# Optimization experiments

Hardware: AMD Instinct MI355X
Metric: run time of the kernel (lower is better)

Reference implementation:

```python
import jax, jax.numpy as jnp
import numpy as np

N_USERS, N_ITEMS, N_ENT = 2500, 3000, 2500
N = N_USERS + N_ITEMS + N_ENT
D, NREL, L, K, NH = 128, 32, 2, 16, 2
NE = 256_000
F_MOVIE, F_USER = 768, 512
GATE_T = 0.5


def _lin(x, w, b):
    return x @ w + b


def setup_inputs() -> dict:
    key = jax.random.key(0)
    ks = iter(jax.random.split(key, 64))
    def rn(shape, s=0.05):
        return jax.random.normal(next(ks), shape, jnp.float32) * s
    def zb():
        return jnp.zeros((D,), jnp.float32)
    inp = dict(
        user_w=rn((N_USERS, D), 0.1), item_w=rn((N_ITEMS, D), 0.1),
        ent_w=rn((N_ENT, D), 0.1), rel_w=rn((NREL, D), 0.1),
        mfeat=rn((N_ITEMS, F_MOVIE), 1.0), ufeat=rn((N_USERS, F_USER), 1.0),
        me_w1=rn((F_MOVIE, D)), me_b1=zb(), me_w2=rn((D, D)), me_b2=zb(),
        ue_w1=rn((F_USER, D)), ue_b1=zb(), ue_w2=rn((D, D)), ue_b2=zb(),
        cm_qw=rn((D, D)), cm_qb=zb(), cm_kw=rn((D, D)), cm_kb=zb(),
        cm_vw=rn((D, D)), cm_vb=zb(), cm_ow=rn((D, D)), cm_ob=zb(),
        mg_w=rn((2 * D, D)), mg_b=zb(), ug_w=rn((2 * D, D)), ug_b=zb(),
        gnn_qw=rn((L, D, D)), gnn_qb=jnp.zeros((L, D), jnp.float32),
        gnn_kw=rn((L, D, D)), gnn_kb=jnp.zeros((L, D), jnp.float32),
        gnn_vw=rn((L, D, D)), gnn_vb=jnp.zeros((L, D), jnp.float32),
        la_w=rn(((L + 1) * D, D)), la_b=zb(),
        adj_data=jax.random.uniform(next(ks), (NE,), jnp.float32, 1e-3, 1.0),
        adj_row=jax.random.randint(next(ks), (NE,), 0, N),
        adj_col=jax.random.randint(next(ks), (NE,), 0, N),
    )
    return inp


def _forward(user_w, item_w, ent_w, rel_w, mfeat, ufeat,
             me_w1, me_b1, me_w2, me_b2, ue_w1, ue_b1, ue_w2, ue_b2,
             cm_qw, cm_qb, cm_kw, cm_kb, cm_vw, cm_vb, cm_ow, cm_ob,
             mg_w, mg_b, ug_w, ug_b,
             gnn_qw, gnn_qb, gnn_kw, gnn_kb, gnn_vw, gnn_vb,
             la_w, la_b, adj_data, adj_row, adj_col):
    hd = D // NH
    # --- modality encoders (dropout is inference-mode identity) ---
    mm_item = jax.nn.relu(_lin(jax.nn.relu(_lin(mfeat, me_w1, me_b1)), me_w2, me_b2))
    mm_user = jax.nn.relu(_lin(jax.nn.relu(_lin(ufeat, ue_w1, ue_b1)), ue_w2, ue_b2))
    # --- MultiHeadCrossModalAttention(mm_item, mm_item): 2 modalities ---
    x = jnp.stack([mm_item, mm_item], axis=1)                     # [B, 2, D]
    B, M = x.shape[0], x.shape[1]
    q = _lin(x, cm_qw, cm_qb).reshape(B, M, NH, hd).transpose(0, 2, 1, 3)
    k = _lin(x, cm_kw, cm_kb).reshape(B, M, NH, hd).transpose(0, 2, 1, 3)
    v = _lin(x, cm_vw, cm_vb).reshape(B, M, NH, hd).transpose(0, 2, 1, 3)
    attn = jax.nn.softmax(jnp.einsum('bhmd,bhnd->bhmn', q, k) / jnp.sqrt(jnp.float32(hd)), axis=-1)
    ao = jnp.einsum('bhmn,bhnd->bhmd', attn, v).transpose(0, 2, 1, 3).reshape(B, M, D)
    mm_item = _lin(ao, cm_ow, cm_ob).sum(axis=1)                  # [B, D]
    # --- gated fusion (NOTE: double sigmoid, faithful to source) ---
    mg = jax.nn.sigmoid(jax.nn.sigmoid(_lin(jnp.concatenate([item_w, mm_item], axis=-1), mg_w, mg_b)) / GATE_T)
    fused_item = mg * item_w + (1.0 - mg) * mm_item + 0.1 * item_w
    ug = jax.nn.sigmoid(jax.nn.sigmoid(_lin(jnp.concatenate([user_w, mm_user], axis=-1), ug_w, ug_b)) / GATE_T)
    fused_user = ug * user_w + (1.0 - ug) * mm_user + 0.1 * user_w
    # --- GNN propagation with SparseKnowledgeAttention ---
    emb = jnp.concatenate([fused_user, fused_item, ent_w], axis=0)  # [N, D]
    rel_mean = rel_w.mean(axis=0)                                  # [D]
    embs = [emb]
    for l in range(L):
        e = embs[-1]
        # sparse adj @ e via gather + segment_sum
        side = jax.ops.segment_sum(adj_data[:, None] * e[adj_col], adj_row, num_segments=N)
        qn = _lin(e, gnn_qw[l], gnn_qb[l])
        kn = _lin(side * rel_mean[None, :], gnn_kw[l], gnn_kb[l])
        scores = (qn @ kn.T) / jnp.sqrt(jnp.float32(D))            # [N, N]
        tv, ti = jax.lax.top_k(scores, K)                          # [N, K]
        w = jax.nn.softmax(tv, axis=-1)
        vn = _lin(side, gnn_vw[l], gnn_vb[l])
        agg = jnp.einsum('nk,nkd->nd', w, vn[ti])                  # gather + weighted sum
        embs.append(jax.nn.relu(agg))
    final = _lin(jnp.concatenate(embs, axis=-1), la_w, la_b)       # layer_agg on stacked layers
    def _norm(z):
        return z / jnp.maximum(jnp.linalg.norm(z, axis=1, keepdims=True), 1e-12)
    return (_norm(final[:N_USERS]),
            _norm(final[N_USERS:N_USERS + N_ITEMS]),
            item_w, mm_item)


def reference(user_w, item_w, ent_w, rel_w, mfeat, ufeat,
              me_w1, me_b1, me_w2, me_b2, ue_w1, ue_b1, ue_w2, ue_b2,
              cm_qw, cm_qb, cm_kw, cm_kb, cm_vw, cm_vb, cm_ow, cm_ob,
              mg_w, mg_b, ug_w, ug_b,
              gnn_qw, gnn_qb, gnn_kw, gnn_kb, gnn_vw, gnn_vb,
              la_w, la_b, adj_data, adj_row, adj_col):
    return _forward(user_w, item_w, ent_w, rel_w, mfeat, ufeat,
                    me_w1, me_b1, me_w2, me_b2, ue_w1, ue_b1, ue_w2, ue_b2,
                    cm_qw, cm_qb, cm_kw, cm_kb, cm_vw, cm_vb, cm_ow, cm_ob,
                    mg_w, mg_b, ug_w, ug_b,
                    gnn_qw, gnn_qb, gnn_kw, gnn_kb, gnn_vw, gnn_vb,
                    la_w, la_b, adj_data, adj_row, adj_col)
```

## Files before the change

kernel.cpp:

```cpp
#include <hip/hip_runtime.h>
#include <hip/hip_bf16.h>
#include <math.h>

#define N_USERS 2500
#define N_ITEMS 3000
#define N_ENT   2500
#define NTOT    8000
#define D       128
#define NEDGE   256000
#define NSLICE  8
#define NMAT    12

typedef unsigned short u16;
typedef unsigned int u32;
typedef unsigned long long u64;
typedef __attribute__((ext_vector_type(8))) short short8;
typedef __attribute__((ext_vector_type(4))) float f32x4;

static __device__ __forceinline__ u16 bf16bits(float x) {
  __hip_bfloat16 h = __float2bfloat16(x);
  return *reinterpret_cast<u16*>(&h);
}

struct WsplitArgs {
  const float* w[NMAT];
  int useks[NMAT];
  int K[NMAT];
  int cum[NMAT + 1];
  int ofs[NMAT];
};

__global__ void k_wsplit_all(WsplitArgs a, const float* __restrict__ relmean,
                             u16* __restrict__ arena) {
  const int e = blockIdx.x * 256 + threadIdx.x;
  if (e >= a.cum[NMAT]) return;
  int i = 0;
  while (e >= a.cum[i + 1]) ++i;
  const int local = e - a.cum[i];
  const int k = local >> 7, j = local & 127;
  const int K = a.K[i];
  float x = a.w[i][(size_t)k * 128 + j];
  if (a.useks[i]) x *= relmean[k];
  const __hip_bfloat16 h1 = __float2bfloat16(x);
  const float r1 = x - __bfloat162float(h1);
  const __hip_bfloat16 h2 = __float2bfloat16(r1);
  const float r2 = r1 - __bfloat162float(h2);
  const __hip_bfloat16 h3 = __float2bfloat16(r2);
  u16* __restrict__ base = arena + a.ofs[i] + (size_t)j * K + k;
  base[0]               = *(const u16*)&h1;
  base[(size_t)128 * K] = *(const u16*)&h2;
  base[(size_t)256 * K] = *(const u16*)&h3;
}

static __device__ __forceinline__ void gemm3_core(const float* __restrict__ A,
                                                  const u16* __restrict__ wsg,
                                                  const float* __restrict__ b,
                                                  float* __restrict__ out,
                                                  u16* __restrict__ ob,
                                                  int M, int K, int mode,
                                                  int bid, int tid) {
  const int lane = tid & 63;
  const int wave = tid >> 6;
  const int rbase = bid * 64 + wave * 16;
  const int colL = lane & 15;
  const int kofs = (lane >> 4) * 8;

  f32x4 acc[8];
#pragma unroll
  for (int ct = 0; ct < 8; ++ct) acc[ct] = (f32x4){0.f, 0.f, 0.f, 0.f};

  const int arow = (rbase + colL < M) ? (rbase + colL) : (M - 1);
  const float* __restrict__ arp = A + (size_t)arow * K;

  for (int k0 = 0; k0 < K; k0 += 32) {
    const float4 f0 = *(const float4*)(arp + k0 + kofs);
    const float4 f1 = *(const float4*)(arp + k0 + kofs + 4);
    float av[8] = {f0.x, f0.y, f0.z, f0.w, f1.x, f1.y, f1.z, f1.w};
    short8 a1, a2, a3;
#pragma unroll
    for (int e = 0; e < 8; ++e) {
      const float x = av[e];
      const __hip_bfloat16 h1 = __float2bfloat16(x);
      const float r1 = x - __bfloat162float(h1);
      const __hip_bfloat16 h2 = __float2bfloat16(r1);
      const float r2 = r1 - __bfloat162float(h2);
      const __hip_bfloat16 h3 = __float2bfloat16(r2);
      a1[e] = *(const short*)&h1;
      a2[e] = *(const short*)&h2;
      a3[e] = *(const short*)&h3;
    }
#pragma unroll
    for (int ct = 0; ct < 8; ++ct) {
      const int j = ct * 16 + colL;
      const u16* wp = wsg + (size_t)j * K + k0 + kofs;
      const short8 b1 = *(const short8*)wp;
      const short8 b2 = *(const short8*)(wp + (size_t)128 * K);
      const short8 b3 = *(const short8*)(wp + (size_t)256 * K);
      acc[ct] = __builtin_amdgcn_mfma_f32_16x16x32_bf16(a1, b1, acc[ct], 0, 0, 0);
      acc[ct] = __builtin_amdgcn_mfma_f32_16x16x32_bf16(a1, b2, acc[ct], 0, 0, 0);
      acc[ct] = __builtin_amdgcn_mfma_f32_16x16x32_bf16(a2, b1, acc[ct], 0, 0, 0);
      acc[ct] = __builtin_amdgcn_mfma_f32_16x16x32_bf16(a2, b2, acc[ct], 0, 0, 0);
      acc[ct] = __builtin_amdgcn_mfma_f32_16x16x32_bf16(a1, b3, acc[ct], 0, 0, 0);
      acc[ct] = __builtin_amdgcn_mfma_f32_16x16x32_bf16(a3, b1, acc[ct], 0, 0, 0);
    }
  }

#pragma unroll
  for (int ct = 0; ct < 8; ++ct) {
    const int j = ct * 16 + colL;
    const float bj = b[j];
#pragma unroll
    for (int r = 0; r < 4; ++r) {
      const int row = rbase + (lane >> 4) * 4 + r;
      if (row < M) {
        float c = acc[ct][r] + bj;
        if (mode == 1) c = fmaxf(c, 0.f);
        else if (mode == 2) c *= 2.f;
        out[(size_t)row * 128 + j] = c;
        if (ob) ob[(size_t)row * 128 + j] = bf16bits(c);
      }
    }
  }
}

static __device__ __forceinline__ void gemm3x2_core(const float* __restrict__ A,
                                                    const u16* __restrict__ wsgA,
                                                    const float* __restrict__ bA,
                                                    float* __restrict__ outA,
                                                    u16* __restrict__ obA,
                                                    const u16* __restrict__ wsgB,
                                                    const float* __restrict__ bB,
                                                    float* __restrict__ outB,
                                                    int M, int K, int bid, int tid) {
  const int lane = tid & 63;
  const int wave = tid >> 6;
  const int rbase = bid * 64 + wave * 16;
  const int colL = lane & 15;
  const int kofs = (lane >> 4) * 8;

  f32x4 accA[8], accB[8];
#pragma unroll
  for (int ct = 0; ct < 8; ++ct) {
    accA[ct] = (f32x4){0.f, 0.f, 0.f, 0.f};
    accB[ct] = (f32x4){0.f, 0.f, 0.f, 0.f};
  }

  const int arow = (rbase + colL < M) ? (rbase + colL) : (M - 1);
  const float* __restrict__ arp = A + (size_t)arow * K;

  for (int k0 = 0; k0 < K; k0 += 32) {
    const float4 f0 = *(const float4*)(arp + k0 + kofs);
    const float4 f1 = *(const float4*)(arp + k0 + kofs + 4);
    float av[8] = {f0.x, f0.y, f0.z, f0.w, f1.x, f1.y, f1.z, f1.w};
    short8 a1, a2, a3;
#pragma unroll
    for (int e = 0; e < 8; ++e) {
      const float x = av[e];
      const __hip_bfloat16 h1 = __float2bfloat16(x);
      const float r1 = x - __bfloat162float(h1);
      const __hip_bfloat16 h2 = __float2bfloat16(r1);
      const float r2 = r1 - __bfloat162float(h2);
      const __hip_bfloat16 h3 = __float2bfloat16(r2);
      a1[e] = *(const short*)&h1;
      a2[e] = *(const short*)&h2;
      a3[e] = *(const short*)&h3;
    }
#pragma unroll
    for (int ct = 0; ct < 8; ++ct) {
      const int j = ct * 16 + colL;
      {
        const u16* wp = wsgA + (size_t)j * K + k0 + kofs;
        const short8 b1 = *(const short8*)wp;
        const short8 b2 = *(const short8*)(wp + (size_t)128 * K);
        const short8 b3 = *(const short8*)(wp + (size_t)256 * K);
        accA[ct] = __builtin_amdgcn_mfma_f32_16x16x32_bf16(a1, b1, accA[ct], 0, 0, 0);
        accA[ct] = __builtin_amdgcn_mfma_f32_16x16x32_bf16(a1, b2, accA[ct], 0, 0, 0);
        accA[ct] = __builtin_amdgcn_mfma_f32_16x16x32_bf16(a2, b1, accA[ct], 0, 0, 0);
        accA[ct] = __builtin_amdgcn_mfma_f32_16x16x32_bf16(a2, b2, accA[ct], 0, 0, 0);
        accA[ct] = __builtin_amdgcn_mfma_f32_16x16x32_bf16(a1, b3, accA[ct], 0, 0, 0);
        accA[ct] = __builtin_amdgcn_mfma_f32_16x16x32_bf16(a3, b1, accA[ct], 0, 0, 0);
      }
      {
        const u16* wp = wsgB + (size_t)j * K + k0 + kofs;
        const short8 b1 = *(const short8*)wp;
        const short8 b2 = *(const short8*)(wp + (size_t)128 * K);
        const short8 b3 = *(const short8*)(wp + (size_t)256 * K);
        accB[ct] = __builtin_amdgcn_mfma_f32_16x16x32_bf16(a1, b1, accB[ct], 0, 0, 0);
        accB[ct] = __builtin_amdgcn_mfma_f32_16x16x32_bf16(a1, b2, accB[ct], 0, 0, 0);
        accB[ct] = __builtin_amdgcn_mfma_f32_16x16x32_bf16(a2, b1, accB[ct], 0, 0, 0);
        accB[ct] = __builtin_amdgcn_mfma_f32_16x16x32_bf16(a2, b2, accB[ct], 0, 0, 0);
        accB[ct] = __builtin_amdgcn_mfma_f32_16x16x32_bf16(a1, b3, accB[ct], 0, 0, 0);
        accB[ct] = __builtin_amdgcn_mfma_f32_16x16x32_bf16(a3, b1, accB[ct], 0, 0, 0);
      }
    }
  }

#pragma unroll
  for (int ct = 0; ct < 8; ++ct) {
    const int j = ct * 16 + colL;
    const float bjA = bA[j];
    const float bjB = bB[j];
#pragma unroll
    for (int r = 0; r < 4; ++r) {
      const int row = rbase + (lane >> 4) * 4 + r;
      if (row < M) {
        const float cA = accA[ct][r] + bjA;
        outA[(size_t)row * 128 + j] = cA;
        obA[(size_t)row * 128 + j] = bf16bits(cA);
        outB[(size_t)row * 128 + j] = accB[ct][r] + bjB;
      }
    }
  }
}

__global__ __launch_bounds__(256) void k_gemm3(const float* __restrict__ A,
                                               const u16* __restrict__ wsg,
                                               const float* __restrict__ b,
                                               float* __restrict__ out,
                                               u16* __restrict__ ob,
                                               int M, int K, int mode) {
  gemm3_core(A, wsg, b, out, ob, M, K, mode, blockIdx.x, threadIdx.x);
}

__global__ __launch_bounds__(256) void k_gemm3b(const float* A0, const u16* w0,
                                                const float* b0, float* o0, int M0, int K0, int nb0,
                                                const float* A1, const u16* w1,
                                                const float* b1, float* o1, int M1, int K1,
                                                int mode) {
  if ((int)blockIdx.x < nb0)
    gemm3_core(A0, w0, b0, o0, nullptr, M0, K0, mode, blockIdx.x, threadIdx.x);
  else
    gemm3_core(A1, w1, b1, o1, nullptr, M1, K1, mode, blockIdx.x - nb0, threadIdx.x);
}

__global__ __launch_bounds__(256) void k_gemm3qkv(const float* e, const u16* wq,
                                                  const float* bq, float* qn, u16* qb,
                                                  const float* side, const u16* wk,
                                                  const float* bk, float* kn, u16* kb,
                                                  const u16* wv, const float* bv, float* vn,
                                                  int M, int nb0) {
  if ((int)blockIdx.x < nb0)
    gemm3_core(e, wq, bq, qn, qb, M, 128, 0, blockIdx.x, threadIdx.x);
  else
    gemm3x2_core(side, wk, bk, kn, kb, wv, bv, vn, M, 128, blockIdx.x - nb0, threadIdx.x);
}

static __device__ __forceinline__ void gemm3w_core(const float* __restrict__ A,
                                                   const u16* __restrict__ wsg,
                                                   const float* __restrict__ b,
                                                   float* __restrict__ out,
                                                   int M, int K, int mode,
                                                   int bid, int tid) {
  const int lane = tid & 63;
  const int wave = tid >> 6;
  const int rbase = bid * 32 + (wave & 1) * 16;
  const int ct0  = (wave >> 1) * 4;
  const int colL = lane & 15;
  const int kofs = (lane >> 4) * 8;

  f32x4 acc[4];
#pragma unroll
  for (int ct = 0; ct < 4; ++ct) acc[ct] = (f32x4){0.f, 0.f, 0.f, 0.f};

  const int arow = (rbase + colL < M) ? (rbase + colL) : (M - 1);
  const float* __restrict__ arp = A + (size_t)arow * K;

  for (int k0 = 0; k0 < K; k0 += 32) {
    const float4 f0 = *(const float4*)(arp + k0 + kofs);
    const float4 f1 = *(const float4*)(arp + k0 + kofs + 4);
    float av[8] = {f0.x, f0.y, f0.z, f0.w, f1.x, f1.y, f1.z, f1.w};
    short8 a1, a2, a3;
#pragma unroll
    for (int e = 0; e < 8; ++e) {
      const float x = av[e];
      const __hip_bfloat16 h1 = __float2bfloat16(x);
      const float r1 = x - __bfloat162float(h1);
      const __hip_bfloat16 h2 = __float2bfloat16(r1);
      const float r2 = r1 - __bfloat162float(h2);
      const __hip_bfloat16 h3 = __float2bfloat16(r2);
      a1[e] = *(const short*)&h1;
      a2[e] = *(const short*)&h2;
      a3[e] = *(const short*)&h3;
    }
#pragma unroll
    for (int ct = 0; ct < 4; ++ct) {
      const int j = (ct0 + ct) * 16 + colL;
      const u16* wp = wsg + (size_t)j * K + k0 + kofs;
      const short8 b1 = *(const short8*)wp;
      const short8 b2 = *(const short8*)(wp + (size_t)128 * K);
      const short8 b3 = *(const short8*)(wp + (size_t)256 * K);
      acc[ct] = __builtin_amdgcn_mfma_f32_16x16x32_bf16(a1, b1, acc[ct], 0, 0, 0);
      acc[ct] = __builtin_amdgcn_mfma_f32_16x16x32_bf16(a1, b2, acc[ct], 0, 0, 0);
      acc[ct] = __builtin_amdgcn_mfma_f32_16x16x32_bf16(a2, b1, acc[ct], 0, 0, 0);
      acc[ct] = __builtin_amdgcn_mfma_f32_16x16x32_bf16(a2, b2, acc[ct], 0, 0, 0);
      acc[ct] = __builtin_amdgcn_mfma_f32_16x16x32_bf16(a1, b3, acc[ct], 0, 0, 0);
      acc[ct] = __builtin_amdgcn_mfma_f32_16x16x32_bf16(a3, b1, acc[ct], 0, 0, 0);
    }
  }

#pragma unroll
  for (int ct = 0; ct < 4; ++ct) {
    const int j = (ct0 + ct) * 16 + colL;
    const float bj = b[j];
#pragma unroll
    for (int r = 0; r < 4; ++r) {
      const int row = rbase + (lane >> 4) * 4 + r;
      if (row < M) {
        float c = acc[ct][r] + bj;
        if (mode == 1) c = fmaxf(c, 0.f);
        else if (mode == 2) c *= 2.f;
        out[(size_t)row * 128 + j] = c;
      }
    }
  }
}

__global__ __launch_bounds__(256) void k_gemm3w2(const float* A0, const u16* w0,
                                                 const float* b0, float* o0, int M0, int K0, int nb0,
                                                 const float* A1, const u16* w1,
                                                 const float* b1, float* o1, int M1, int K1,
                                                 int mode) {
  if ((int)blockIdx.x < nb0)
    gemm3w_core(A0, w0, b0, o0, M0, K0, mode, blockIdx.x, threadIdx.x);
  else
    gemm3w_core(A1, w1, b1, o1, M1, K1, mode, blockIdx.x - nb0, threadIdx.x);
}

__global__ void k_gatefuse2(const float* __restrict__ user_w, const float* __restrict__ mm_user,
                            const float* __restrict__ ug_w, const float* __restrict__ ug_b,
                            const float* __restrict__ item_w, const float* __restrict__ mm_item,
                            const float* __restrict__ mg_w, const float* __restrict__ mg_b,
                            float* __restrict__ emb0,
                            const float* __restrict__ ent_w,
                            float* __restrict__ outItem, float* __restrict__ outMM) {
  const int r = blockIdx.x;
  const int j = threadIdx.x;
  if (r >= N_USERS + N_ITEMS) {
    const int t = (r - (N_USERS + N_ITEMS)) * 128 + j;
    if (t < N_ENT * D) emb0[(size_t)(N_USERS + N_ITEMS) * D + t] = ent_w[t];
    outItem[t] = item_w[t];
    outMM[t]   = mm_item[t];
    return;
  }
  const float* b0; const float* m0; const float* gw; const float* gb;
  if (r < N_USERS) {
    b0 = user_w + (size_t)r * D; m0 = mm_user + (size_t)r * D; gw = ug_w; gb = ug_b;
  } else {
    const int ri = r - N_USERS;
    b0 = item_w + (size_t)ri * D; m0 = mm_item + (size_t)ri * D; gw = mg_w; gb = mg_b;
  }
  float acc = 0.f;
  for (int k = 0; k < D; ++k) acc = fmaf(b0[k], gw[(size_t)k * D + j], acc);
  for (int k = 0; k < D; ++k) acc = fmaf(m0[k], gw[(size_t)(D + k) * D + j], acc);
  acc += gb[j];
  const float s1 = 1.f / (1.f + expf(-acc));
  const float g  = 1.f / (1.f + expf(-(s1 * 2.f)));
  const float bv = b0[j], mv = m0[j];
  emb0[(size_t)r * D + j] = g * bv + (1.f - g) * mv + 0.1f * bv;
}

__global__ void k_relmean(const float* __restrict__ rel, float* __restrict__ out) {
  const int j = threadIdx.x;
  float s = 0.f;
  for (int i = 0; i < 32; ++i) s += rel[i * D + j];
  out[j] = s * (1.f / 32.f);
}

__global__ void k_hist(const int* __restrict__ rw, int* __restrict__ cnt) {
  const int e = blockIdx.x * 256 + threadIdx.x;
  if (e < NEDGE) atomicAdd(&cnt[rw[e]], 1);
}

__global__ __launch_bounds__(1024) void k_scan(int* __restrict__ cnt,
                                               int* __restrict__ rowptr,
                                               int* __restrict__ cursor) {
  __shared__ int part[1024];
  const int t = threadIdx.x;
  const int base = t * 8;
  int loc[8];
  int s = 0;
#pragma unroll
  for (int j = 0; j < 8; ++j) {
    const int v = (base + j < NTOT) ? cnt[base + j] : 0;
    loc[j] = s; s += v;
  }
  part[t] = s;
  __syncthreads();
  for (int off = 1; off < 1024; off <<= 1) {
    const int v = (t >= off) ? part[t - off] : 0;
    __syncthreads();
    part[t] += v;
    __syncthreads();
  }
  const int pre = (t == 0) ? 0 : part[t - 1];
#pragma unroll
  for (int j = 0; j < 8; ++j) {
    if (base + j < NTOT) {
      const int p = pre + loc[j];
      rowptr[base + j] = p;
      cursor[base + j] = p;
    }
  }
  if (t == 1023) rowptr[NTOT] = part[1023];
}

__global__ void k_scatter(const int* __restrict__ rw, int* __restrict__ cursor,
                          int* __restrict__ perm) {
  const int e = blockIdx.x * 256 + threadIdx.x;
  if (e >= NEDGE) return;
  const int pos = atomicAdd(&cursor[rw[e]], 1);
  perm[pos] = e;
}

__global__ __launch_bounds__(128) void k_spmm_csr(const float* __restrict__ dat,
                                                  const int* __restrict__ cl,
                                                  const int* __restrict__ perm,
                                                  const int* __restrict__ rowptr,
                                                  const float* __restrict__ emb,
                                                  float* __restrict__ side) {
  const int r = blockIdx.x;
  const int d = threadIdx.x;
  const int beg = rowptr[r], end = rowptr[r + 1];
  float acc = 0.f;
  for (int i = beg; i < end; ++i) {
    const int ei = perm[i];
    acc = fmaf(dat[ei], emb[(size_t)cl[ei] * D + d], acc);
  }
  side[(size_t)r * D + d] = acc;
}

__global__ __launch_bounds__(256) void k_topk6v(const u16* __restrict__ qb,
                                                const u16* __restrict__ kb,
                                                int* __restrict__ cand) {
  __shared__ u64 km[4][8][97];
  const int tid  = threadIdx.x;
  const int lane = tid & 63;
  const int wave = tid >> 6;
  const int rbase = blockIdx.x * 16;
  const int sl   = blockIdx.y * 4 + wave;
  const int colL = lane & 15;
  const int g    = lane >> 4;
  const int kofs = g * 8;

  short8 aF[4];
  {
    const u16* ap = qb + (size_t)(rbase + colL) * D + kofs;
#pragma unroll
    for (int t = 0; t < 4; ++t) aF[t] = *reinterpret_cast<const short8*>(ap + t * 32);
  }

  float s[4][6]; int c[4][6];
#pragma unroll
  for (int r = 0; r < 4; ++r)
#pragma unroll
    for (int j = 0; j < 6; ++j) { s[r][j] = -3.0e38f; c[r][j] = 0x40000000 + colL * 6 + j; }

  const int tile0  = sl * 62 + (sl < 4 ? sl : 4);
  const int ntiles = 62 + (sl < 4 ? 1 : 0);
  const u16* bb = kb + (size_t)(tile0 * 16 + colL) * D + kofs;

  short8 bF[4];
#pragma unroll
  for (int t = 0; t < 4; ++t) bF[t] = *reinterpret_cast<const short8*>(bb + t * 32);

  for (int ct = 0; ct < ntiles; ++ct) {
    const int cn = (ct + 1 < ntiles) ? ct + 1 : ct;
    const u16* nb = bb + (size_t)cn * 16 * D;
    short8 bN[4];
#pragma unroll
    for (int t = 0; t < 4; ++t) bN[t] = *reinterpret_cast<const short8*>(nb + t * 32);

    f32x4 acc = {0.f, 0.f, 0.f, 0.f};
#pragma unroll
    for (int t = 0; t < 4; ++t)
      acc = __builtin_amdgcn_mfma_f32_16x16x32_bf16(aF[t], bF[t], acc, 0, 0, 0);

    const int colIdx = (tile0 + ct) * 16 + colL;
#pragma unroll
    for (int r = 0; r < 4; ++r) {
      float ks = acc[r]; int kc = colIdx;
      if (ks > s[r][5]) {
#pragma unroll
        for (int i = 0; i < 6; ++i) {
          const bool bgt = ks > s[r][i];
          const float os = s[r][i]; const int oc = c[r][i];
          s[r][i] = bgt ? ks : os;  c[r][i] = bgt ? kc : oc;
          ks      = bgt ? os : ks;  kc      = bgt ? oc : kc;
        }
      }
    }

#pragma unroll
    for (int t = 0; t < 4; ++t) bF[t] = bN[t];
  }

  u64 kk[4][6];
#pragma unroll
  for (int r = 0; r < 4; ++r)
#pragma unroll
    for (int j = 0; j < 6; ++j) {
      const u32 b = __builtin_bit_cast(u32, s[r][j]);
      const u32 mono = b ^ ((u32)(((int)b) >> 31) | 0x80000000u);
      kk[r][j] = ((u64)mono << 32) | (u64)(0xFFFFFFFFu - (u32)c[r][j]);
    }

  if (g < 2) {
#pragma unroll
    for (int r = 0; r < 4; ++r)
#pragma unroll
      for (int j = 0; j < 6; ++j)
        km[wave][4 * g + r][colL * 6 + j] = kk[r][j];
  }
  __syncthreads();
  if (g < 2) {
#pragma unroll
    for (int r = 0; r < 4; ++r) {
      int cnt[6] = {0, 0, 0, 0, 0, 0};
      for (int q2 = 0; q2 < 96; ++q2) {
        const u64 o = km[wave][4 * g + r][q2];
#pragma unroll
        for (int j = 0; j < 6; ++j) cnt[j] += (o > kk[r][j]) ? 1 : 0;
      }
      const int row = rbase + 4 * g + r;
#pragma unroll
      for (int j = 0; j < 6; ++j)
        if (cnt[j] < 16)
          cand[(size_t)row * 128 + sl * 16 + cnt[j]] = c[r][j];
    }
  }
  __syncthreads();
  if (g >= 2) {
#pragma unroll
    for (int r = 0; r < 4; ++r)
#pragma unroll
      for (int j = 0; j < 6; ++j)
        km[wave][4 * (g - 2) + r][colL * 6 + j] = kk[r][j];
  }
  __syncthreads();
  if (g >= 2) {
#pragma unroll
    for (int r = 0; r < 4; ++r) {
      int cnt[6] = {0, 0, 0, 0, 0, 0};
      for (int q2 = 0; q2 < 96; ++q2) {
        const u64 o = km[wave][4 * (g - 2) + r][q2];
#pragma unroll
        for (int j = 0; j < 6; ++j) cnt[j] += (o > kk[r][j]) ? 1 : 0;
      }
      const int row = rbase + 4 * g + r;
#pragma unroll
      for (int j = 0; j < 6; ++j)
        if (cnt[j] < 16)
          cand[(size_t)row * 128 + sl * 16 + cnt[j]] = c[r][j];
    }
  }
}

__global__ __launch_bounds__(64) void k_rescore128(const float* __restrict__ qn,
                                                   const float* __restrict__ kn,
                                                   const float* __restrict__ vn,
                                                   const int* __restrict__ cand,
                                                   float* __restrict__ enext) {
  __shared__ u64 skey[128];
  const int row = blockIdx.x;
  const int lane = threadIdx.x;
  const int* cr = cand + (size_t)row * 128;
  const int c0 = cr[lane];
  const int c1 = cr[64 + lane];

  const float4* __restrict__ q4  = (const float4*)(qn + (size_t)row * D);
  const float4* __restrict__ k40 = (const float4*)(kn + (size_t)c0 * D);
  const float4* __restrict__ k41 = (const float4*)(kn + (size_t)c1 * D);
  float s0 = 0.f, s1 = 0.f;
#pragma unroll 8
  for (int j = 0; j < 32; ++j) {
    const float4 qv = q4[j];
    const float4 a = k40[j], b = k41[j];
    s0 = fmaf(qv.x, a.x, s0); s0 = fmaf(qv.y, a.y, s0);
    s0 = fmaf(qv.z, a.z, s0); s0 = fmaf(qv.w, a.w, s0);
    s1 = fmaf(qv.x, b.x, s1); s1 = fmaf(qv.y, b.y, s1);
    s1 = fmaf(qv.z, b.z, s1); s1 = fmaf(qv.w, b.w, s1);
  }
  const float inv = 0.088388347648318447f;
  s0 *= inv; s1 *= inv;

  const u32 b0i = __builtin_bit_cast(u32, s0);
  const u32 b1i = __builtin_bit_cast(u32, s1);
  const u64 key0 = ((u64)(b0i ^ ((u32)(((int)b0i) >> 31) | 0x80000000u)) << 32)
                   | (u64)(0xFFFFFFFFu - (u32)c0);
  const u64 key1 = ((u64)(b1i ^ ((u32)(((int)b1i) >> 31) | 0x80000000u)) << 32)
                   | (u64)(0xFFFFFFFFu - (u32)c1);
  skey[lane] = key0;
  skey[64 + lane] = key1;
  __syncthreads();

  int r0 = 0, r1 = 0;
#pragma unroll 8
  for (int j = 0; j < 128; ++j) {
    const u64 o = skey[j];
    r0 += (o > key0) ? 1 : 0;
    r1 += (o > key1) ? 1 : 0;
  }
  const bool sel0 = r0 < 16, sel1 = r1 < 16;

  float v = fmaxf(sel0 ? s0 : -3.0e38f, sel1 ? s1 : -3.0e38f);
#pragma unroll
  for (int d2 = 1; d2 < 64; d2 <<= 1) v = fmaxf(v, __shfl_xor(v, d2));
  const float e0 = sel0 ? expf(s0 - v) : 0.f;
  const float e1 = sel1 ? expf(s1 - v) : 0.f;
  float Z = e0 + e1;
#pragma unroll
  for (int d2 = 1; d2 < 64; d2 <<= 1) Z += __shfl_xor(Z, d2);
  const float w0 = e0 / Z, w1 = e1 / Z;

  float a0 = 0.f, a1 = 0.f;
  unsigned long long bm0 = __ballot(sel0);
  while (bm0) {
    const int src = __ffsll(bm0) - 1; bm0 &= bm0 - 1;
    const float wj = __shfl(w0, src);
    const int   cj = __shfl(c0, src);
    const float* __restrict__ vr = vn + (size_t)cj * D;
    a0 = fmaf(wj, vr[lane], a0);
    a1 = fmaf(wj, vr[64 + lane], a1);
  }
  unsigned long long bm1 = __ballot(sel1);
  while (bm1) {
    const int src = __ffsll(bm1) - 1; bm1 &= bm1 - 1;
    const float wj = __shfl(w1, src);
    const int   cj = __shfl(c1, src);
    const float* __restrict__ vr = vn + (size_t)cj * D;
    a0 = fmaf(wj, vr[lane], a0);
    a1 = fmaf(wj, vr[64 + lane], a1);
  }
  enext[(size_t)row * D + lane]      = fmaxf(a0, 0.f);
  enext[(size_t)row * D + 64 + lane] = fmaxf(a1, 0.f);
}

__global__ void k_final_norm(const float* __restrict__ e0, const float* __restrict__ e1,
                             const float* __restrict__ e2, const float* __restrict__ law,
                             const float* __restrict__ lab, float* __restrict__ out) {
  __shared__ float red[128];
  const int r = blockIdx.x;
  const int j = threadIdx.x;
  const float* __restrict__ a0 = e0 + (size_t)r * D;
  const float* __restrict__ a1 = e1 + (size_t)r * D;
  const float* __restrict__ a2 = e2 + (size_t)r * D;
  float acc = lab[j];
  for (int k = 0; k < D; ++k) acc = fmaf(a0[k], law[(size_t)k * D + j], acc);
  for (int k = 0; k < D; ++k) acc = fmaf(a1[k], law[(size_t)(D + k) * D + j], acc);
  for (int k = 0; k < D; ++k) acc = fmaf(a2[k], law[(size_t)(2 * D + k) * D + j], acc);
  red[j] = acc * acc;
  __syncthreads();
  for (int st = 64; st > 0; st >>= 1) {
    if (j < st) red[j] += red[j + st];
    __syncthreads();
  }
  const float nrm = fmaxf(sqrtf(red[0]), 1e-12f);
  const float o = acc / nrm;
  if (r < N_USERS) out[(size_t)r * D + j] = o;
  else             out[(size_t)N_USERS * D + (size_t)(r - N_USERS) * D + j] = o;
}

extern "C" void kernel_launch(void* const* d_in, const int* in_sizes, int n_in,
                              void* d_out, int out_size, void* d_ws, size_t ws_size,
                              hipStream_t stream) {
  const float* user_w = (const float*)d_in[0];
  const float* item_w = (const float*)d_in[1];
  const float* ent_w  = (const float*)d_in[2];
  const float* rel_w  = (const float*)d_in[3];
  const float* mfeat  = (const float*)d_in[4];
  const float* ufeat  = (const float*)d_in[5];
  const float* me_w1  = (const float*)d_in[6];
  const float* me_b1  = (const float*)d_in[7];
  const float* me_w2  = (const float*)d_in[8];
  const float* me_b2  = (const float*)d_in[9];
  const float* ue_w1  = (const float*)d_in[10];
  const float* ue_b1  = (const float*)d_in[11];
  const float* ue_w2  = (const float*)d_in[12];
  const float* ue_b2  = (const float*)d_in[13];
  const float* cm_vw  = (const float*)d_in[18];
  const float* cm_vb  = (const float*)d_in[19];
  const float* cm_ow  = (const float*)d_in[20];
  const float* cm_ob  = (const float*)d_in[21];
  const float* mg_w   = (const float*)d_in[22];
  const float* mg_b   = (const float*)d_in[23];
  const float* ug_w   = (const float*)d_in[24];
  const float* ug_b   = (const float*)d_in[25];
  const float* gnn_qw = (const float*)d_in[26];
  const float* gnn_qb = (const float*)d_in[27];
  const float* gnn_kw = (const float*)d_in[28];
  const float* gnn_kb = (const float*)d_in[29];
  const float* gnn_vw = (const float*)d_in[30];
  const float* gnn_vb = (const float*)d_in[31];
  const float* la_w   = (const float*)d_in[32];
  const float* la_b   = (const float*)d_in[33];
  const float* adj_d  = (const float*)d_in[34];
  const int*   adj_r  = (const int*)d_in[35];
  const int*   adj_c  = (const int*)d_in[36];
  float* out = (float*)d_out;
  float* ws  = (float*)d_ws;

  size_t off = 0;
  float* mm_item = ws + off; off += (size_t)N_ITEMS * D;
  float* mm_user = ws + off; off += (size_t)N_USERS * D;
  float* enc     = ws + off; off += (size_t)N_ITEMS * D;
  float* tmp     = ws + off; off += (size_t)N_ITEMS * D;
  float* emb0    = ws + off; off += (size_t)NTOT * D;
  float* emb1    = ws + off; off += (size_t)NTOT * D;
  float* emb2    = ws + off; off += (size_t)NTOT * D;
  float* side    = ws + off; off += (size_t)NTOT * D;
  float* qn      = ws + off; off += (size_t)NTOT * D;
  float* kn      = ws + off; off += (size_t)NTOT * D;
  float* vn      = ws + off; off += (size_t)NTOT * D;
  float* relmean = ws + off; off += D;
  u16* arena = (u16*)(ws + off); off += 491520;
  u16* qb = (u16*)mm_user;
  u16* kb = qb + (size_t)NTOT * D;
  int* cand = (int*)side;
  int* rowptr = (int*)emb2;
  int* cursor = rowptr + 8064;
  int* permB  = cursor + 8064;
  float* utmp = side;

  static const int Ks[NMAT]  = {768, 128, 512, 128, 128, 128, 128, 128, 128, 128, 128, 128};
  int ofs[NMAT], cum[NMAT + 1];
  {
    int o = 0, cc = 0;
    for (int i = 0; i < NMAT; ++i) {
      ofs[i] = o; o += 3 * Ks[i] * 128;
      cum[i] = cc; cc += Ks[i] * 128;
    }
    cum[NMAT] = cc;
  }

  WsplitArgs wa;
  const float* wptr[NMAT] = {me_w1, me_w2, ue_w1, ue_w2, cm_vw, cm_ow,
                             gnn_qw, gnn_kw, gnn_vw,
                             gnn_qw + (size_t)D * D, gnn_kw + (size_t)D * D,
                             gnn_vw + (size_t)D * D};
  for (int i = 0; i < NMAT; ++i) {
    wa.w[i] = wptr[i];
    wa.useks[i] = (i == 7 || i == 10) ? 1 : 0;
    wa.K[i] = Ks[i];
    wa.cum[i] = cum[i];
    wa.ofs[i] = ofs[i];
  }
  wa.cum[NMAT] = cum[NMAT];

  k_relmean<<<1, D, 0, stream>>>(rel_w, relmean);
  k_wsplit_all<<<(cum[NMAT] + 255) / 256, 256, 0, stream>>>(wa, relmean, arena);

  const int nbI1 = (3000 + 31) / 32;
  const int nbU1 = (2500 + 31) / 32;
  k_gemm3w2<<<nbI1 + nbU1, 256, 0, stream>>>(
      mfeat, arena + ofs[0], me_b1, tmp,  3000, 768, nbI1,
      ufeat, arena + ofs[2], ue_b1, utmp, 2500, 512, 1);
  const int nbI2 = (3000 + 63) / 64;
  const int nbU2 = (2500 + 63) / 64;
  k_gemm3b<<<nbI2 + nbU2, 256, 0, stream>>>(
      tmp,  arena + ofs[1], me_b2, enc,     3000, 128, nbI2,
      utmp, arena + ofs[3], ue_b2, mm_user, 2500, 128, 1);
  k_gemm3<<<(3000 + 63) / 64, 256, 0, stream>>>(enc, arena + ofs[4], cm_vb, tmp, nullptr, 3000, 128, 0);
  k_gemm3<<<(3000 + 63) / 64, 256, 0, stream>>>(tmp, arena + ofs[5], cm_ob, mm_item, nullptr, 3000, 128, 2);
  k_gatefuse2<<<N_USERS + N_ITEMS + 3000, D, 0, stream>>>(
      user_w, mm_user, ug_w, ug_b, item_w, mm_item, mg_w, mg_b, emb0,
      ent_w,
      out + (size_t)(N_USERS + N_ITEMS) * D,
      out + (size_t)(N_USERS + 2 * N_ITEMS) * D);

  hipMemsetAsync(cursor, 0, NTOT * sizeof(int), stream);
  k_hist<<<(NEDGE + 255) / 256, 256, 0, stream>>>(adj_r, cursor);
  k_scan<<<1, 1024, 0, stream>>>(cursor, rowptr, cursor);
  k_scatter<<<(NEDGE + 255) / 256, 256, 0, stream>>>(adj_r, cursor, permB);

  const float* eml[3] = {emb0, emb1, emb2};
  for (int l = 0; l < 2; ++l) {
    const float* e = eml[l];
    float* enext   = (float*)eml[l + 1];
    k_spmm_csr<<<NTOT, 128, 0, stream>>>(adj_d, adj_c, permB, rowptr, e, side);
    const int nbq = (NTOT + 63) / 64;
    k_gemm3qkv<<<2 * nbq, 256, 0, stream>>>(
        e, arena + ofs[6 + 3 * l], gnn_qb + (size_t)l * D, qn, qb,
        side, arena + ofs[7 + 3 * l], gnn_kb + (size_t)l * D, kn, kb,
        arena + ofs[8 + 3 * l], gnn_vb + (size_t)l * D, vn,
        NTOT, nbq);
    dim3 tkgrid(NTOT / 16, 2);
    k_topk6v<<<tkgrid, 256, 0, stream>>>(qb, kb, cand);
    k_rescore128<<<NTOT, 64, 0, stream>>>(qn, kn, vn, cand, enext);
  }

  k_final_norm<<<N_USERS + N_ITEMS, D, 0, stream>>>(emb0, emb1, emb2, la_w, la_b, out);
}
```

Measured before the change: 920.2 us.

## Use split-bf16 MFMA for final layer-agg, fuse relmean, unroll SpMM

Replaces the scalar per-row final layer-aggregation and L2-normalize kernel with an MFMA kernel. The kernel splits activations and weights into three bf16 parts to approximate fp32 accuracy, and computes the row norm with lane shuffles. The la_w weight is added to the pre-split arena. The separate relmean kernel is removed: the relation mean is now recomputed inside the weight-split kernel, which saves a launch but adds redundant reads. The CSR SpMM loop is also unrolled by two with dual accumulators to overlap gathers.

```diff
diff --git a/kernel.cpp b/kernel.cpp
--- a/kernel.cpp
+++ b/kernel.cpp
@@ -9,7 +9,7 @@
 #define D       128
 #define NEDGE   256000
 #define NSLICE  8
-#define NMAT    12
+#define NMAT    13
 
 typedef unsigned short u16;
 typedef unsigned int u32;
@@ -30,7 +30,7 @@
   int ofs[NMAT];
 };
 
-__global__ void k_wsplit_all(WsplitArgs a, const float* __restrict__ relmean,
+__global__ void k_wsplit_all(WsplitArgs a, const float* __restrict__ rel,
                              u16* __restrict__ arena) {
   const int e = blockIdx.x * 256 + threadIdx.x;
   if (e >= a.cum[NMAT]) return;
@@ -40,7 +40,12 @@
   const int k = local >> 7, j = local & 127;
   const int K = a.K[i];
   float x = a.w[i][(size_t)k * 128 + j];
-  if (a.useks[i]) x *= relmean[k];
+  if (a.useks[i]) {
+    float s = 0.f;
+#pragma unroll
+    for (int t = 0; t < 32; ++t) s += rel[t * 128 + k];
+    x *= s * (1.f / 32.f);
+  }
   const __hip_bfloat16 h1 = __float2bfloat16(x);
   const float r1 = x - __bfloat162float(h1);
   const __hip_bfloat16 h2 = __float2bfloat16(r1);
@@ -245,6 +250,97 @@
     gemm3x2_core(side, wk, bk, kn, kb, wv, bv, vn, M, 128, blockIdx.x - nb0, threadIdx.x);
 }
 
+__global__ __launch_bounds__(256) void k_gemm3norm(const float* __restrict__ e0,
+                                                   const float* __restrict__ e1,
+                                                   const float* __restrict__ e2,
+                                                   const u16* __restrict__ wsg,
+                                                   const float* __restrict__ lab,
+                                                   float* __restrict__ out) {
+  const int tid  = threadIdx.x;
+  const int lane = tid & 63;
+  const int wave = tid >> 6;
+  const int rbase = blockIdx.x * 64 + wave * 16;
+  const int colL = lane & 15;
+  const int kofs = (lane >> 4) * 8;
+  const int M = N_USERS + N_ITEMS;
+  const int K = 384;
+
+  f32x4 acc[8];
+#pragma unroll
+  for (int ct = 0; ct < 8; ++ct) acc[ct] = (f32x4){0.f, 0.f, 0.f, 0.f};
+
+  const int arow = (rbase + colL < M) ? (rbase + colL) : (M - 1);
+
+#pragma unroll
+  for (int k0 = 0; k0 < 384; k0 += 32) {
+    const float* __restrict__ src =
+        (k0 < 128) ? (e0 + (size_t)arow * 128 + k0)
+      : (k0 < 256) ? (e1 + (size_t)arow * 128 + (k0 - 128))
+                   : (e2 + (size_t)arow * 128 + (k0 - 256));
+    const float4 f0 = *(const float4*)(src + kofs);
+    const float4 f1 = *(const float4*)(src + kofs + 4);
+    float av[8] = {f0.x, f0.y, f0.z, f0.w, f1.x, f1.y, f1.z, f1.w};
+    short8 a1, a2, a3;
+#pragma unroll
+    for (int e = 0; e < 8; ++e) {
+      const float x = av[e];
+      const __hip_bfloat16 h1 = __float2bfloat16(x);
+      const float r1 = x - __bfloat162float(h1);
+      const __hip_bfloat16 h2 = __float2bfloat16(r1);
+      const float r2 = r1 - __bfloat162float(h2);
+      const __hip_bfloat16 h3 = __float2bfloat16(r2);
+      a1[e] = *(const short*)&h1;
+      a2[e] = *(const short*)&h2;
+      a3[e] = *(const short*)&h3;
+    }
+#pragma unroll
+    for (int ct = 0; ct < 8; ++ct) {
+      const int j = ct * 16 + colL;
+      const u16* wp = wsg + (size_t)j * K + k0 + kofs;
+      const short8 b1 = *(const short8*)wp;
+      const short8 b2 = *(const short8*)(wp + (size_t)128 * K);
+      const short8 b3 = *(const short8*)(wp + (size_t)256 * K);
+      acc[ct] = __builtin_amdgcn_mfma_f32_16x16x32_bf16(a1, b1, acc[ct], 0, 0, 0);
+      acc[ct] = __builtin_amdgcn_mfma_f32_16x16x32_bf16(a1, b2, acc[ct], 0, 0, 0);
+      acc[ct] = __builtin_amdgcn_mfma_f32_16x16x32_bf16(a2, b1, acc[ct], 0, 0, 0);
+      acc[ct] = __builtin_amdgcn_mfma_f32_16x16x32_bf16(a2, b2, acc[ct], 0, 0, 0);
+      acc[ct] = __builtin_amdgcn_mfma_f32_16x16x32_bf16(a1, b3, acc[ct], 0, 0, 0);
+      acc[ct] = __builtin_amdgcn_mfma_f32_16x16x32_bf16(a3, b1, acc[ct], 0, 0, 0);
+    }
+  }
+
+  float val[8][4];
+  float ss[4] = {0.f, 0.f, 0.f, 0.f};
+#pragma unroll
+  for (int ct = 0; ct < 8; ++ct) {
+    const float bj = lab[ct * 16 + colL];
+#pragma unroll
+    for (int r = 0; r < 4; ++r) {
+      const float v = acc[ct][r] + bj;
+      val[ct][r] = v;
+      ss[r] = fmaf(v, v, ss[r]);
+    }
+  }
+#pragma unroll
+  for (int r = 0; r < 4; ++r) {
+    float t = ss[r];
+    t += __shfl_xor(t, 1);
+    t += __shfl_xor(t, 2);
+    t += __shfl_xor(t, 4);
+    t += __shfl_xor(t, 8);
+    ss[r] = fmaxf(sqrtf(t), 1e-12f);
+  }
+#pragma unroll
+  for (int ct = 0; ct < 8; ++ct) {
+    const int j = ct * 16 + colL;
+#pragma unroll
+    for (int r = 0; r < 4; ++r) {
+      const int row = rbase + (lane >> 4) * 4 + r;
+      if (row < M) out[(size_t)row * 128 + j] = val[ct][r] / ss[r];
+    }
+  }
+}
+
 static __device__ __forceinline__ void gemm3w_core(const float* __restrict__ A,
                                                    const u16* __restrict__ wsg,
                                                    const float* __restrict__ b,
@@ -359,13 +455,6 @@
   emb0[(size_t)r * D + j] = g * bv + (1.f - g) * mv + 0.1f * bv;
 }
 
-__global__ void k_relmean(const float* __restrict__ rel, float* __restrict__ out) {
-  const int j = threadIdx.x;
-  float s = 0.f;
-  for (int i = 0; i < 32; ++i) s += rel[i * D + j];
-  out[j] = s * (1.f / 32.f);
-}
-
 __global__ void k_hist(const int* __restrict__ rw, int* __restrict__ cnt) {
   const int e = blockIdx.x * 256 + threadIdx.x;
   if (e < NEDGE) atomicAdd(&cnt[rw[e]], 1);
@@ -421,12 +510,19 @@
   const int r = blockIdx.x;
   const int d = threadIdx.x;
   const int beg = rowptr[r], end = rowptr[r + 1];
-  float acc = 0.f;
-  for (int i = beg; i < end; ++i) {
-    const int ei = perm[i];
-    acc = fmaf(dat[ei], emb[(size_t)cl[ei] * D + d], acc);
-  }
-  side[(size_t)r * D + d] = acc;
+  float acc0 = 0.f, acc1 = 0.f;
+  int i = beg;
+  for (; i + 1 < end; i += 2) {
+    const int e0 = perm[i];
+    const int e1 = perm[i + 1];
+    acc0 = fmaf(dat[e0], emb[(size_t)cl[e0] * D + d], acc0);
+    acc1 = fmaf(dat[e1], emb[(size_t)cl[e1] * D + d], acc1);
+  }
+  if (i < end) {
+    const int e0 = perm[i];
+    acc0 = fmaf(dat[e0], emb[(size_t)cl[e0] * D + d], acc0);
+  }
+  side[(size_t)r * D + d] = acc0 + acc1;
 }
 
 __global__ __launch_bounds__(256) void k_topk6v(const u16* __restrict__ qb,
@@ -633,31 +729,6 @@
   }
   enext[(size_t)row * D + lane]      = fmaxf(a0, 0.f);
   enext[(size_t)row * D + 64 + lane] = fmaxf(a1, 0.f);
-}
-
-__global__ void k_final_norm(const float* __restrict__ e0, const float* __restrict__ e1,
-                             const float* __restrict__ e2, const float* __restrict__ law,
-                             const float* __restrict__ lab, float* __restrict__ out) {
-  __shared__ float red[128];
-  const int r = blockIdx.x;
-  const int j = threadIdx.x;
-  const float* __restrict__ a0 = e0 + (size_t)r * D;
-  const float* __restrict__ a1 = e1 + (size_t)r * D;
-  const float* __restrict__ a2 = e2 + (size_t)r * D;
-  float acc = lab[j];
-  for (int k = 0; k < D; ++k) acc = fmaf(a0[k], law[(size_t)k * D + j], acc);
-  for (int k = 0; k < D; ++k) acc = fmaf(a1[k], law[(size_t)(D + k) * D + j], acc);
-  for (int k = 0; k < D; ++k) acc = fmaf(a2[k], law[(size_t)(2 * D + k) * D + j], acc);
-  red[j] = acc * acc;
-  __syncthreads();
-  for (int st = 64; st > 0; st >>= 1) {
-    if (j < st) red[j] += red[j + st];
-    __syncthreads();
-  }
-  const float nrm = fmaxf(sqrtf(red[0]), 1e-12f);
-  const float o = acc / nrm;
-  if (r < N_USERS) out[(size_t)r * D + j] = o;
-  else             out[(size_t)N_USERS * D + (size_t)(r - N_USERS) * D + j] = o;
 }
 
 extern "C" void kernel_launch(void* const* d_in, const int* in_sizes, int n_in,
@@ -711,8 +782,8 @@
   float* qn      = ws + off; off += (size_t)NTOT * D;
   float* kn      = ws + off; off += (size_t)NTOT * D;
   float* vn      = ws + off; off += (size_t)NTOT * D;
-  float* relmean = ws + off; off += D;
-  u16* arena = (u16*)(ws + off); off += 491520;
+  off += D;
+  u16* arena = (u16*)(ws + off); off += 565248;
   u16* qb = (u16*)mm_user;
   u16* kb = qb + (size_t)NTOT * D;
   int* cand = (int*)side;
@@ -721,7 +792,7 @@
   int* permB  = cursor + 8064;
   float* utmp = side;
 
-  static const int Ks[NMAT]  = {768, 128, 512, 128, 128, 128, 128, 128, 128, 128, 128, 128};
+  static const int Ks[NMAT]  = {768, 128, 512, 128, 128, 128, 128, 128, 128, 128, 128, 128, 384};
   int ofs[NMAT], cum[NMAT + 1];
   {
     int o = 0, cc = 0;
@@ -736,7 +807,7 @@
   const float* wptr[NMAT] = {me_w1, me_w2, ue_w1, ue_w2, cm_vw, cm_ow,
                              gnn_qw, gnn_kw, gnn_vw,
                              gnn_qw + (size_t)D * D, gnn_kw + (size_t)D * D,
-                             gnn_vw + (size_t)D * D};
+                             gnn_vw + (size_t)D * D, la_w};
   for (int i = 0; i < NMAT; ++i) {
     wa.w[i] = wptr[i];
     wa.useks[i] = (i == 7 || i == 10) ? 1 : 0;
@@ -746,8 +817,7 @@
   }
   wa.cum[NMAT] = cum[NMAT];
 
-  k_relmean<<<1, D, 0, stream>>>(rel_w, relmean);
-  k_wsplit_all<<<(cum[NMAT] + 255) / 256, 256, 0, stream>>>(wa, relmean, arena);
+  k_wsplit_all<<<(cum[NMAT] + 255) / 256, 256, 0, stream>>>(wa, rel_w, arena);
 
   const int nbI1 = (3000 + 31) / 32;
   const int nbU1 = (2500 + 31) / 32;
@@ -788,5 +858,6 @@
     k_rescore128<<<NTOT, 64, 0, stream>>>(qn, kn, vn, cand, enext);
   }
 
-  k_final_norm<<<N_USERS + N_ITEMS, D, 0, stream>>>(emb0, emb1, emb2, la_w, la_b, out);
-}
+  k_gemm3norm<<<(N_USERS + N_ITEMS + 63) / 64, 256, 0, stream>>>(
+      emb0, emb1, emb2, arena + ofs[12], la_b, out);
+}
```

Measured after the change: 925.8 us. About the same (+0.6%).
